# Performance work log

Measured on AMD Instinct MI355X. Metric: run time of the kernel, lower is better.

## Reference

```python
import math
import jax, jax.numpy as jnp
import numpy as np

D_MODEL = 1024
L_MAX = 4096
BATCH = 2
FILTER_ORDER = 64
EMB_DIM = 3


def _make_z(L, emb_dim=EMB_DIM):
    # PositionalEmbedding: [time, real bands, imag bands] -> [1, L, emb_dim]
    t = jnp.linspace(0.0, 1.0, L)[None, :, None]
    bands = (emb_dim - 1) // 2
    t_res = jnp.linspace(0.0, L - 1.0, L)[None, :, None]
    w = 2.0 * math.pi * t_res / L
    f = jnp.linspace(1e-4, float(bands - 1), bands)[None, None]
    ph = f * w  # z = exp(-1j*ph) -> real=cos(ph), imag=-sin(ph)
    return jnp.concatenate([t, jnp.cos(ph), -jnp.sin(ph)], axis=-1).astype(jnp.float32)


def setup_inputs() -> dict:
    key = jax.random.key(0)
    ks = jax.random.split(key, 16)
    d = D_MODEL
    iw = 3 * d  # inner_width = d_model * (order + 1), order=2

    def rn(k, shape, scale):
        return (jax.random.normal(k, shape) * scale).astype(jnp.float32)

    return {
        'u': rn(ks[0], (BATCH, L_MAX, d), 1.0),
        'w_in': rn(ks[1], (iw, d), d ** -0.5),
        'b_in': rn(ks[2], (iw,), 0.01),
        'sf_w': rn(ks[3], (iw, 1, 3), 3 ** -0.5),
        'sf_b': rn(ks[4], (iw,), 0.01),
        'z': _make_z(L_MAX),
        'w0': rn(ks[5], (FILTER_ORDER, EMB_DIM), EMB_DIM ** -0.5),
        'b0': rn(ks[6], (FILTER_ORDER,), 0.01),
        'freq': jnp.ones((1, FILTER_ORDER), dtype=jnp.float32),  # Sin(w=1)
        'w1': rn(ks[7], (FILTER_ORDER, FILTER_ORDER), FILTER_ORDER ** -0.5),
        'b1': rn(ks[8], (FILTER_ORDER,), 0.01),
        'w2': rn(ks[9], (FILTER_ORDER, FILTER_ORDER), FILTER_ORDER ** -0.5),
        'b2': rn(ks[10], (FILTER_ORDER,), 0.01),
        'wf': rn(ks[11], (d, FILTER_ORDER), FILTER_ORDER ** -0.5),
        'D': rn(ks[12], (d,), 1.0),
        'w_out': rn(ks[13], (d, d), d ** -0.5),
        'b_out': rn(ks[14], (d,), 0.01),
    }


def _dwconv(x, w, b):
    # depthwise Conv1d(kernel=3, padding=2, groups=C); x: [B, C, L] -> [B, C, L+2]
    y = jax.lax.conv_general_dilated(
        x, w, window_strides=(1,), padding=[(2, 2)],
        feature_group_count=x.shape[1],
        dimension_numbers=('NCH', 'OIH', 'NCH'))
    return y + b[None, :, None]


def _fftconv(v, k, D):
    # circular conv via zero-padded FFT; torch's k_f/fft_size with norm='forward'
    # irfft cancels to the standard (norm='backward') inverse.
    L = v.shape[-1]
    n = 2 * L
    y = jnp.fft.irfft(jnp.fft.rfft(v, n=n) * jnp.fft.rfft(k, n=n), n=n)[..., :L]
    return y + v * D[:, None]


def reference(u, w_in, b_in, sf_w, sf_b, z, w0, b0, freq, w1, b1, w2, b2, wf, D, w_out, b_out):
    b, l, d = u.shape
    L = min(l, L_MAX)

    # input projection + short depthwise filter
    up = jnp.einsum('bld,ed->ble', u, w_in) + b_in  # [b, l, 3d]
    up = up.transpose(0, 2, 1)                       # [b, 3d, l]
    uc = _dwconv(up, sf_w, sf_b)[..., :L]            # [b, 3d, L]
    x0, x1, v = jnp.split(uc, 3, axis=1)             # each [b, d, L]

    # implicit filter MLP with shared Sin activation
    h = jnp.sin(freq * (z @ w0.T + b0))              # [1, L, 64]
    h = jnp.sin(freq * (h @ w1.T + b1))
    h = jnp.sin(freq * (h @ w2.T + b2))
    h = h @ wf.T                                     # [1, L, d]

    # exponential modulation (buffers: t, deltas)
    t = jnp.linspace(0.0, 1.0, L)[None, :, None]
    max_decay = math.log(0.01) / 0.3
    min_decay = math.log(0.01) / 1.5
    deltas = jnp.linspace(min_decay, max_decay, d)[None, None]
    h = h * jnp.exp(-t * jnp.abs(deltas))            # [1, L, d]
    k = h[0].T                                       # [d, L]

    # hyena recurrence (order=2 -> one gated fft conv)
    v = _fftconv(v * x1, k, D)
    y = (v * x0).transpose(0, 2, 1)                  # [b, L, d]
    return jnp.einsum('bld,ed->ble', y, w_out) + b_out
```

## Files before the change

kernel.cpp:

```cpp
#include <hip/hip_runtime.h>
#include <math.h>

#define DM   1024
#define LL   4096
#define NB   2
#define E3   3072
#define FPI  3.14159265358979323846f

typedef __bf16 bf16x8 __attribute__((ext_vector_type(8)));
typedef float  f32x4  __attribute__((ext_vector_type(4)));
typedef _Float16 f16x2 __attribute__((ext_vector_type(2)));

__device__ __forceinline__ unsigned short f2bf(float x) {
    unsigned u = __float_as_uint(x);
    u += 0x7fffu + ((u >> 16) & 1u);
    return (unsigned short)(u >> 16);
}
__device__ __forceinline__ float bf2f(ushort s) {
    return __uint_as_float(((unsigned)s) << 16);
}
__device__ __forceinline__ void gload16(void* lds, const void* g) {
    typedef const __attribute__((address_space(1))) unsigned int* gp_t;
    typedef __attribute__((address_space(3))) unsigned int* lp_t;
    __builtin_amdgcn_global_load_lds((gp_t)g, (lp_t)lds, 16, 0, 0);
}

__global__ __launch_bounds__(256) void k_cvt3(
    const float* __restrict__ a, ushort* __restrict__ oa, int n4a,
    const float* __restrict__ b, ushort* __restrict__ ob, int n4b,
    const float* __restrict__ c, ushort* __restrict__ oc, int n4c)
{
    int idx = blockIdx.x * 256 + threadIdx.x;
    int stride = gridDim.x * 256;
    int tot = n4a + n4b + n4c;
    for (int i = idx; i < tot; i += stride) {
        const float4* src; ushort* dst; int k;
        if (i < n4a)            { src = (const float4*)a; dst = oa; k = i; }
        else if (i < n4a + n4b) { src = (const float4*)b; dst = ob; k = i - n4a; }
        else                    { src = (const float4*)c; dst = oc; k = i - n4a - n4b; }
        float4 v = src[k];
        ushort4 o;
        o.x = f2bf(v.x); o.y = f2bf(v.y); o.z = f2bf(v.z); o.w = f2bf(v.w);
        *reinterpret_cast<ushort4*>(dst + 4 * k) = o;
    }
}

__global__ __launch_bounds__(512, 1) void k_gemm128n(
    const ushort* __restrict__ A, const ushort* __restrict__ B,
    const float* __restrict__ bias, ushort* __restrict__ C,
    int Ntiles, int ldc)
{
    __shared__ __align__(16) char ldsm[98304];
    const int tid  = threadIdx.x;
    const int lane = tid & 63;
    const int w    = tid >> 6;
    const int wr   = w >> 2, wc = w & 3;

    const int nch = Ntiles >> 3;
    const int xcd = blockIdx.x & 7;
    const int loc = blockIdx.x >> 3;
    const int n0 = ((xcd * nch) + (loc % nch)) << 8;
    const int m0 = (loc / nch) << 7;

    const int r0 = tid >> 2;
    const int swzc = ((tid & 3) ^ ((r0 >> 1) & 3)) << 4;
    const char* Asrc = (const char*)A + ((size_t)(m0 + r0) << 11) + swzc;
    const char* Bsrc = (const char*)B + ((size_t)(n0 + r0) << 11) + swzc;
    char* Ld = ldsm + tid * 16;

    const int lm = lane & 15, lk = lane >> 4;
    const int rA = wr * 64 + lm;
    const int rB = wc * 64 + lm;
    const int aBase = rA * 64 + ((lk ^ ((rA >> 1) & 3)) << 4);
    const int bBase = 16384 + rB * 64 + ((lk ^ ((rB >> 1) & 3)) << 4);

#define STG_A(ks, nb, t1) \
    gload16(Ld + (nb) + (ks)*8192, Asrc + (t1)*128 + (ks)*64)
#define STG_B(ks, nb, t1) do { \
    gload16(Ld + (nb) + 16384 + (ks)*16384,        Bsrc + (t1)*128 + (ks)*64); \
    gload16(Ld + (nb) + 16384 + (ks)*16384 + 8192, Bsrc + (t1)*128 + (ks)*64 + 262144); } while(0)
#define LDA(buf, ks, m) (*(const bf16x8*)(ldsm + (buf) + (ks)*8192 + aBase + (m)*1024))
#define LDB(buf, ks, n) (*(const bf16x8*)(ldsm + (buf) + (ks)*16384 + bBase + (n)*1024))
#define VMCNT3() asm volatile("s_waitcnt vmcnt(3)" ::: "memory")
#define VMCNT0() asm volatile("s_waitcnt vmcnt(0)" ::: "memory")
#define BAR() __builtin_amdgcn_s_barrier()

    f32x4 acc[4][4];
#pragma unroll
    for (int i = 0; i < 4; ++i)
#pragma unroll
        for (int j = 0; j < 4; ++j)
#pragma unroll
            for (int r = 0; r < 4; ++r) acc[i][j][r] = 0.f;

    STG_A(0, 0, 0); STG_B(0, 0, 0); STG_A(1, 0, 0); STG_B(1, 0, 0);
    VMCNT3();
    BAR();

    bf16x8 af[2], bq[4];
#pragma unroll 1
    for (int t = 0; t < 15; ++t) {
        const int buf = (t & 1) * 49152;
        const int nb  = 49152 - buf;
        const int t1  = t + 1;
#pragma unroll
        for (int n = 0; n < 4; ++n) bq[n] = LDB(buf, 0, n);
        af[0] = LDA(buf, 0, 0); af[1] = LDA(buf, 0, 1);
        STG_A(0, nb, t1);
        BAR();
        __builtin_amdgcn_s_setprio(1);
#pragma unroll
        for (int m = 0; m < 2; ++m)
#pragma unroll
            for (int n = 0; n < 4; ++n)
                acc[m][n] = __builtin_amdgcn_mfma_f32_16x16x32_bf16(af[m], bq[n], acc[m][n], 0, 0, 0);
        __builtin_amdgcn_s_setprio(0);
        BAR();
        af[0] = LDA(buf, 0, 2); af[1] = LDA(buf, 0, 3);
        STG_B(0, nb, t1);
        VMCNT3();
        BAR();
        __builtin_amdgcn_s_setprio(1);
#pragma unroll
        for (int m = 0; m < 2; ++m)
#pragma unroll
            for (int n = 0; n < 4; ++n)
                acc[2 + m][n] = __builtin_amdgcn_mfma_f32_16x16x32_bf16(af[m], bq[n], acc[2 + m][n], 0, 0, 0);
        __builtin_amdgcn_s_setprio(0);
        BAR();
#pragma unroll
        for (int n = 0; n < 4; ++n) bq[n] = LDB(buf, 1, n);
        af[0] = LDA(buf, 1, 0); af[1] = LDA(buf, 1, 1);
        STG_A(1, nb, t1);
        BAR();
        __builtin_amdgcn_s_setprio(1);
#pragma unroll
        for (int m = 0; m < 2; ++m)
#pragma unroll
            for (int n = 0; n < 4; ++n)
                acc[m][n] = __builtin_amdgcn_mfma_f32_16x16x32_bf16(af[m], bq[n], acc[m][n], 0, 0, 0);
        __builtin_amdgcn_s_setprio(0);
        BAR();
        af[0] = LDA(buf, 1, 2); af[1] = LDA(buf, 1, 3);
        STG_B(1, nb, t1);
        VMCNT3();
        BAR();
        __builtin_amdgcn_s_setprio(1);
#pragma unroll
        for (int m = 0; m < 2; ++m)
#pragma unroll
            for (int n = 0; n < 4; ++n)
                acc[2 + m][n] = __builtin_amdgcn_mfma_f32_16x16x32_bf16(af[m], bq[n], acc[2 + m][n], 0, 0, 0);
        __builtin_amdgcn_s_setprio(0);
        BAR();
    }
    {
        const int buf = 49152;
#pragma unroll
        for (int n = 0; n < 4; ++n) bq[n] = LDB(buf, 0, n);
        af[0] = LDA(buf, 0, 0); af[1] = LDA(buf, 0, 1);
#pragma unroll
        for (int m = 0; m < 2; ++m)
#pragma unroll
            for (int n = 0; n < 4; ++n)
                acc[m][n] = __builtin_amdgcn_mfma_f32_16x16x32_bf16(af[m], bq[n], acc[m][n], 0, 0, 0);
        af[0] = LDA(buf, 0, 2); af[1] = LDA(buf, 0, 3);
#pragma unroll
        for (int m = 0; m < 2; ++m)
#pragma unroll
            for (int n = 0; n < 4; ++n)
                acc[2 + m][n] = __builtin_amdgcn_mfma_f32_16x16x32_bf16(af[m], bq[n], acc[2 + m][n], 0, 0, 0);
        VMCNT0();
        BAR();
#pragma unroll
        for (int n = 0; n < 4; ++n) bq[n] = LDB(buf, 1, n);
        af[0] = LDA(buf, 1, 0); af[1] = LDA(buf, 1, 1);
#pragma unroll
        for (int m = 0; m < 2; ++m)
#pragma unroll
            for (int n = 0; n < 4; ++n)
                acc[m][n] = __builtin_amdgcn_mfma_f32_16x16x32_bf16(af[m], bq[n], acc[m][n], 0, 0, 0);
        af[0] = LDA(buf, 1, 2); af[1] = LDA(buf, 1, 3);
#pragma unroll
        for (int m = 0; m < 2; ++m)
#pragma unroll
            for (int n = 0; n < 4; ++n)
                acc[2 + m][n] = __builtin_amdgcn_mfma_f32_16x16x32_bf16(af[m], bq[n], acc[2 + m][n], 0, 0, 0);
    }
    const int er = lk << 2, ec = lm;
#pragma unroll
    for (int m = 0; m < 4; ++m) {
        int row = m0 + wr * 64 + m * 16 + er;
#pragma unroll
        for (int n = 0; n < 4; ++n) {
            int col = n0 + wc * 64 + n * 16 + ec;
            ushort* cp = C + (size_t)row * ldc + col;
#pragma unroll
            for (int r = 0; r < 4; ++r)
                cp[(size_t)r * ldc] = f2bf(acc[m][n][r] + bias[row + r]);
        }
    }
#undef STG_A
#undef STG_B
#undef LDA
#undef LDB
#undef VMCNT3
#undef VMCNT0
#undef BAR
}

__global__ __launch_bounds__(256) void k_gemm_bf16(
    const ushort* __restrict__ A, const ushort* __restrict__ B,
    const float* __restrict__ bias, float* __restrict__ C, int ldc)
{
    __shared__ ushort As[128 * 32];
    __shared__ ushort Bs[128 * 32];
    const int tid  = threadIdx.x;
    const int lane = tid & 63;
    const int w    = tid >> 6;
    const int wm   = (w >> 1) << 6, wn = (w & 1) << 6;
    const int m0   = blockIdx.y << 7, n0 = blockIdx.x << 7;

    f32x4 acc[4][4];
#pragma unroll
    for (int i = 0; i < 4; ++i)
#pragma unroll
        for (int j = 0; j < 4; ++j)
#pragma unroll
            for (int r = 0; r < 4; ++r) acc[i][j][r] = 0.f;

    const char* Ab = (const char*)A + ((size_t)(m0 + (tid >> 2)) << 11) + ((tid & 3) << 4);
    const char* Bb = (const char*)B + ((size_t)(n0 + (tid >> 2)) << 11) + ((tid & 3) << 4);
    char* AsD = (char*)As + tid * 16;
    char* BsD = (char*)Bs + tid * 16;
    const char* ap = (const char*)As + ((wm + (lane & 15)) << 6) + ((lane >> 4) << 4);
    const char* bp = (const char*)Bs + ((wn + (lane & 15)) << 6) + ((lane >> 4) << 4);

    for (int k0 = 0; k0 < 1024; k0 += 32) {
        __syncthreads();
        gload16(AsD,        Ab + k0 * 2);
        gload16(AsD + 4096, Ab + 131072 + k0 * 2);
        gload16(BsD,        Bb + k0 * 2);
        gload16(BsD + 4096, Bb + 131072 + k0 * 2);
        __syncthreads();
        bf16x8 af[4], bfr[4];
#pragma unroll
        for (int i = 0; i < 4; ++i) {
            af[i]  = *(const bf16x8*)(ap + (i << 10));
            bfr[i] = *(const bf16x8*)(bp + (i << 10));
        }
#pragma unroll
        for (int i = 0; i < 4; ++i)
#pragma unroll
            for (int j = 0; j < 4; ++j)
                acc[i][j] = __builtin_amdgcn_mfma_f32_16x16x32_bf16(
                    af[i], bfr[j], acc[i][j], 0, 0, 0);
    }
    const int er = (lane >> 4) << 2;
    const int ec = lane & 15;
#pragma unroll
    for (int i = 0; i < 4; ++i) {
        int row = m0 + wm + (i << 4) + er;
#pragma unroll
        for (int j = 0; j < 4; ++j) {
            int col = n0 + wn + (j << 4) + ec;
            float bz = bias[col];
            float* cp = C + (size_t)row * ldc + col;
#pragma unroll
            for (int r = 0; r < 4; ++r)
                cp[(size_t)r * ldc] = acc[i][j][r] + bz;
        }
    }
}

__global__ __launch_bounds__(256) void k_filt_mlp(
    const float* __restrict__ z, const float* __restrict__ w0,
    const float* __restrict__ b0, const float* __restrict__ fr,
    const float* __restrict__ w1, const float* __restrict__ b1,
    const float* __restrict__ w2, const float* __restrict__ b2,
    float* __restrict__ H3)
{
    __shared__ float w1t[64 * 65];
    __shared__ float w2t[64 * 65];
    __shared__ float hb[4][64];
    const int tid = threadIdx.x;
    for (int idx = tid; idx < 4096; idx += 256) {
        int j = idx >> 6, m = idx & 63;
        w1t[m*65 + j] = w1[idx];
        w2t[m*65 + j] = w2[idx];
    }
    __syncthreads();
    const int tl = tid >> 6, j = tid & 63;
    const float frj = fr[j];
    const float b0j = b0[j], b1j = b1[j], b2j = b2[j];
    const float w00 = w0[j*3+0], w01 = w0[j*3+1], w02 = w0[j*3+2];
    const int t0 = blockIdx.x * 16;
    for (int r = 0; r < 4; ++r) {
        int t = t0 + r*4 + tl;
        float z0 = z[t*3+0], z1 = z[t*3+1], z2 = z[t*3+2];
        float h = sinf(frj * (b0j + z0*w00 + z1*w01 + z2*w02));
        hb[tl][j] = h;
        __syncthreads();
        float s = b1j;
#pragma unroll
        for (int m = 0; m < 64; ++m) s = fmaf(hb[tl][m], w1t[m*65 + j], s);
        __syncthreads();
        h = sinf(frj * s);
        hb[tl][j] = h;
        __syncthreads();
        s = b2j;
#pragma unroll
        for (int m = 0; m < 64; ++m) s = fmaf(hb[tl][m], w2t[m*65 + j], s);
        h = sinf(frj * s);
        H3[(size_t)t * 64 + j] = h;
        __syncthreads();
    }
}

__global__ __launch_bounds__(256) void k_filt_k(
    const float* __restrict__ H3, const float* __restrict__ wf,
    float* __restrict__ kf)
{
    __shared__ float Hs[64][65];
    __shared__ float Ws[64][65];
    const int tid = threadIdx.x;
    const int t0 = blockIdx.x * 64, d0 = blockIdx.y * 64;
    for (int idx = tid; idx < 4096; idx += 256) {
        int r = idx >> 6, cc = idx & 63;
        Hs[r][cc] = H3[(size_t)(t0 + r) * 64 + cc];
        Ws[r][cc] = wf[(size_t)(d0 + r) * 64 + cc];
    }
    __syncthreads();
    const int tx = tid & 15, ty = tid >> 4;
    float acc[4][4];
#pragma unroll
    for (int i = 0; i < 4; ++i)
#pragma unroll
        for (int jj = 0; jj < 4; ++jj) acc[i][jj] = 0.f;
#pragma unroll
    for (int j = 0; j < 64; ++j) {
        float wv[4], hv[4];
#pragma unroll
        for (int i = 0; i < 4; ++i) wv[i] = Ws[4*ty + i][j];
#pragma unroll
        for (int i = 0; i < 4; ++i) hv[i] = Hs[4*tx + i][j];
#pragma unroll
        for (int i = 0; i < 4; ++i)
#pragma unroll
            for (int jj = 0; jj < 4; ++jj) acc[i][jj] = fmaf(wv[i], hv[jj], acc[i][jj]);
    }
    const float mind = -3.0701134573253944f;
    const float maxd = -15.350567286626972f;
#pragma unroll
    for (int i = 0; i < 4; ++i) {
        int d = d0 + 4*ty + i;
        float delta = fabsf(mind + (maxd - mind) * ((float)d / 1023.f));
#pragma unroll
        for (int jj = 0; jj < 4; ++jj) {
            int t = t0 + 4*tx + jj;
            float tn = (float)t / 4095.f;
            kf[(size_t)d * LL + t] = acc[i][jj] * expf(-tn * delta);
        }
    }
}

__device__ __forceinline__ int pidx(int p) { return p + (p >> 4); }

__device__ __forceinline__ float2 cmul(float2 a, float2 b) {
    return make_float2(a.x*b.x - a.y*b.y, a.x*b.y + a.y*b.x);
}

__device__ void fft_lds_fwd4(float2* buf, int tid) {
    int lh = 10;
#pragma unroll
    for (int h = 2048; h >= 32; h >>= 2, lh -= 2) {
        const int hh = h >> 1;
        const float rinv = -FPI / (float)h;
        __syncthreads();
#pragma unroll
        for (int r = 0; r < 4; ++r) {
            int bf = (r << 9) + tid;
            int q  = bf & (hh - 1);
            int g  = bf >> lh;
            int j  = (g << (lh + 2)) + q;
            float2 a = buf[pidx(j)];
            float2 b = buf[pidx(j + hh)];
            float2 c = buf[pidx(j + h)];
            float2 d = buf[pidx(j + h + hh)];
            float2 t0 = make_float2(a.x + c.x, a.y + c.y);
            float2 t1 = make_float2(a.x - c.x, a.y - c.y);
            float2 t2 = make_float2(b.x + d.x, b.y + d.y);
            float2 t3 = make_float2(b.y - d.y, d.x - b.x);
            float sn, cs;
            __sincosf(rinv * (float)q, &sn, &cs);
            float c2 = cs*cs - sn*sn, s2 = 2.f*cs*sn;
            float c3 = cs*c2 - sn*s2, s3 = cs*s2 + sn*c2;
            buf[pidx(j)] = make_float2(t0.x + t2.x, t0.y + t2.y);
            float2 e1 = make_float2(t0.x - t2.x, t0.y - t2.y);
            buf[pidx(j + hh)] = make_float2(e1.x*c2 - e1.y*s2, e1.x*s2 + e1.y*c2);
            float2 e2 = make_float2(t1.x + t3.x, t1.y + t3.y);
            buf[pidx(j + h)] = make_float2(e2.x*cs - e2.y*sn, e2.x*sn + e2.y*cs);
            float2 e3 = make_float2(t1.x - t3.x, t1.y - t3.y);
            buf[pidx(j + h + hh)] = make_float2(e3.x*c3 - e3.y*s3, e3.x*s3 + e3.y*c3);
        }
    }
    __syncthreads();
}

__device__ void fft_lds_inv4(float2* buf, int tid) {
    int lh = 4;
#pragma unroll
    for (int h = 32; h <= 2048; h <<= 2, lh += 2) {
        const int hh = h >> 1;
        const float rpos = FPI / (float)h;
        __syncthreads();
#pragma unroll
        for (int r = 0; r < 4; ++r) {
            int bf = (r << 9) + tid;
            int q  = bf & (hh - 1);
            int g  = bf >> lh;
            int j  = (g << (lh + 2)) + q;
            float2 o0 = buf[pidx(j)];
            float2 o1 = buf[pidx(j + hh)];
            float2 o2 = buf[pidx(j + h)];
            float2 o3 = buf[pidx(j + h + hh)];
            float sn, cs;
            __sincosf(rpos * (float)q, &sn, &cs);
            float c2 = cs*cs - sn*sn, s2 = 2.f*cs*sn;
            float c3 = cs*c2 - sn*s2, s3 = cs*s2 + sn*c2;
            float2 p1 = make_float2(o1.x*c2 - o1.y*s2, o1.x*s2 + o1.y*c2);
            float2 p2 = make_float2(o2.x*cs - o2.y*sn, o2.x*sn + o2.y*cs);
            float2 p3 = make_float2(o3.x*c3 - o3.y*s3, o3.x*s3 + o3.y*c3);
            float2 u0 = make_float2(o0.x + p1.x, o0.y + p1.y);
            float2 u1 = make_float2(o0.x - p1.x, o0.y - p1.y);
            float2 u2 = make_float2(p2.x + p3.x, p2.y + p3.y);
            float2 u3 = make_float2(p2.x - p3.x, p2.y - p3.y);
            float2 ib = make_float2(-u3.y, u3.x);
            buf[pidx(j)]          = make_float2(u0.x + u2.x, u0.y + u2.y);
            buf[pidx(j + hh)]     = make_float2(u1.x + ib.x, u1.y + ib.y);
            buf[pidx(j + h)]      = make_float2(u0.x - u2.x, u0.y - u2.y);
            buf[pidx(j + h + hh)] = make_float2(u1.x - ib.x, u1.y - ib.y);
        }
    }
    __syncthreads();
}

__device__ __forceinline__ void fft_reg_fwd(float2* c) {
    const float W16r[8] = {1.f, 0.92387953f, 0.70710678f, 0.38268343f,
                           0.f, -0.38268343f, -0.70710678f, -0.92387953f};
    const float W16i[8] = {0.f, -0.38268343f, -0.70710678f, -0.92387953f,
                           -1.f, -0.92387953f, -0.70710678f, -0.38268343f};
#pragma unroll
    for (int k = 0; k < 8; ++k) {
        float2 a = c[k], b = c[k+8];
        float2 d = make_float2(a.x - b.x, a.y - b.y);
        c[k]   = make_float2(a.x + b.x, a.y + b.y);
        c[k+8] = cmul(d, make_float2(W16r[k], W16i[k]));
    }
    const float W8r[4] = {1.f, 0.70710678f, 0.f, -0.70710678f};
    const float W8i[4] = {0.f, -0.70710678f, -1.f, -0.70710678f};
#pragma unroll
    for (int blk = 0; blk < 16; blk += 8)
#pragma unroll
        for (int k = 0; k < 4; ++k) {
            float2 a = c[blk+k], b = c[blk+k+4];
            float2 d = make_float2(a.x - b.x, a.y - b.y);
            c[blk+k]   = make_float2(a.x + b.x, a.y + b.y);
            c[blk+k+4] = cmul(d, make_float2(W8r[k], W8i[k]));
        }
#pragma unroll
    for (int blk = 0; blk < 16; blk += 4) {
        {   float2 a = c[blk], b = c[blk+2];
            c[blk]   = make_float2(a.x + b.x, a.y + b.y);
            c[blk+2] = make_float2(a.x - b.x, a.y - b.y); }
        {   float2 a = c[blk+1], b = c[blk+3];
            float2 d = make_float2(a.x - b.x, a.y - b.y);
            c[blk+1] = make_float2(a.x + b.x, a.y + b.y);
            c[blk+3] = make_float2(d.y, -d.x); }
    }
#pragma unroll
    for (int blk = 0; blk < 16; blk += 2) {
        float2 a = c[blk], b = c[blk+1];
        c[blk]   = make_float2(a.x + b.x, a.y + b.y);
        c[blk+1] = make_float2(a.x - b.x, a.y - b.y);
    }
}

__device__ __forceinline__ void fft_reg_inv(float2* c) {
#pragma unroll
    for (int blk = 0; blk < 16; blk += 2) {
        float2 a = c[blk], b = c[blk+1];
        c[blk]   = make_float2(a.x + b.x, a.y + b.y);
        c[blk+1] = make_float2(a.x - b.x, a.y - b.y);
    }
#pragma unroll
    for (int blk = 0; blk < 16; blk += 4) {
        {   float2 a = c[blk], b = c[blk+2];
            c[blk]   = make_float2(a.x + b.x, a.y + b.y);
            c[blk+2] = make_float2(a.x - b.x, a.y - b.y); }
        {   float2 a = c[blk+1], b = c[blk+3];
            float2 bt = make_float2(-c[blk+3].y, c[blk+3].x);
            c[blk+1] = make_float2(a.x + bt.x, a.y + bt.y);
            c[blk+3] = make_float2(a.x - bt.x, a.y - bt.y); }
    }
    const float W8r[4] = {1.f, 0.70710678f, 0.f, -0.70710678f};
    const float W8i[4] = {0.f, 0.70710678f, 1.f, 0.70710678f};
#pragma unroll
    for (int blk = 0; blk < 16; blk += 8)
#pragma unroll
        for (int k = 0; k < 4; ++k) {
            float2 a = c[blk+k], b = c[blk+k+4];
            float2 bt = cmul(b, make_float2(W8r[k], W8i[k]));
            c[blk+k]   = make_float2(a.x + bt.x, a.y + bt.y);
            c[blk+k+4] = make_float2(a.x - bt.x, a.y - bt.y);
        }
    const float W16r[8] = {1.f, 0.92387953f, 0.70710678f, 0.38268343f,
                           0.f, -0.38268343f, -0.70710678f, -0.92387953f};
    const float W16i[8] = {0.f, 0.38268343f, 0.70710678f, 0.92387953f,
                           1.f, 0.92387953f, 0.70710678f, 0.38268343f};
#pragma unroll
    for (int k = 0; k < 8; ++k) {
        float2 a = c[k], b = c[k+8];
        float2 bt = cmul(b, make_float2(W16r[k], W16i[k]));
        c[k]   = make_float2(a.x + bt.x, a.y + bt.y);
        c[k+8] = make_float2(a.x - bt.x, a.y - bt.y);
    }
}

__global__ __launch_bounds__(512) void k_kfft(
    const float* __restrict__ kf, f16x2* __restrict__ Kf)
{
    __shared__ float2 buf[8704];
    const int d = blockIdx.x, tid = threadIdx.x;
    const float* krow = kf + (size_t)d * LL;
    const float rinv0 = -FPI / 4096.f;
    for (int i = tid; i < 1024; i += 512) {
        float4 k4 = reinterpret_cast<const float4*>(krow)[i];
        int p = 4 * i;
        float kv[4] = {k4.x, k4.y, k4.z, k4.w};
#pragma unroll
        for (int q = 0; q < 4; ++q) {
            float sn, cs;
            __sincosf(rinv0 * (float)(p + q), &sn, &cs);
            buf[pidx(p + q)]        = make_float2(kv[q], 0.f);
            buf[pidx(p + q + 4096)] = make_float2(kv[q] * cs, kv[q] * sn);
        }
    }
    fft_lds_fwd4(buf, tid);
    float2 c[16];
    const int p0 = tid * 16;
#pragma unroll
    for (int j = 0; j < 16; ++j) c[j] = buf[pidx(p0 + j)];
    fft_reg_fwd(c);
    f16x2* outp = Kf + (size_t)d * 8192 + p0;
#pragma unroll
    for (int j = 0; j < 16; ++j) {
        f16x2 o;
        o[0] = (_Float16)(c[j].x * (1.f/8192.f));
        o[1] = (_Float16)(c[j].y * (1.f/8192.f));
        outp[j] = o;
    }
}

__device__ __forceinline__ void conv4(const ushort* __restrict__ row, int p,
    float w0, float w1, float w2, float bias, float* out)
{
    float xm2, xm1;
    if (p >= 2) {
        unsigned prev = *reinterpret_cast<const unsigned*>(row + p - 2);
        xm2 = bf2f((ushort)(prev & 0xffffu));
        xm1 = bf2f((ushort)(prev >> 16));
    } else { xm2 = 0.f; xm1 = 0.f; }
    uint2 cur = *reinterpret_cast<const uint2*>(row + p);
    float x0 = bf2f((ushort)(cur.x & 0xffffu));
    float x1 = bf2f((ushort)(cur.x >> 16));
    float x2 = bf2f((ushort)(cur.y & 0xffffu));
    float x3 = bf2f((ushort)(cur.y >> 16));
    out[0] = fmaf(w2, x0, fmaf(w1, xm1, fmaf(w0, xm2, bias)));
    out[1] = fmaf(w2, x1, fmaf(w1, x0,  fmaf(w0, xm1, bias)));
    out[2] = fmaf(w2, x2, fmaf(w1, x1,  fmaf(w0, x0,  bias)));
    out[3] = fmaf(w2, x3, fmaf(w1, x2,  fmaf(w0, x1,  bias)));
}

__global__ __launch_bounds__(512) void k_fftconv(
    const ushort* __restrict__ up2, const f16x2* __restrict__ Kf,
    const float* __restrict__ sfw, const float* __restrict__ sfb,
    const float* __restrict__ Dp, ushort* __restrict__ yg)
{
    __shared__ float2 buf[8704];
    const int d = blockIdx.x, tid = threadIdx.x;
    const ushort* vrow0  = up2 + (size_t)(2048 + d) * 8192;
    const ushort* vrow1  = vrow0 + 4096;
    const ushort* x1row0 = up2 + (size_t)(1024 + d) * 8192;
    const ushort* x1row1 = x1row0 + 4096;
    const ushort* x0row0 = up2 + (size_t)d * 8192;
    const ushort* x0row1 = x0row0 + 4096;
    const float wv0 = sfw[(2048+d)*3+0], wv1 = sfw[(2048+d)*3+1],
                wv2 = sfw[(2048+d)*3+2], bv = sfb[2048+d];
    const float wx0 = sfw[(1024+d)*3+0], wx1 = sfw[(1024+d)*3+1],
                wx2 = sfw[(1024+d)*3+2], bx = sfb[1024+d];
    const float g0 = sfw[d*3+0], g1 = sfw[d*3+1], g2 = sfw[d*3+2], bg = sfb[d];
    const float rinv0 = -FPI / 4096.f;

    float vs0[8], vs1[8];
#pragma unroll
    for (int ii = 0; ii < 2; ++ii) {
        int p = 4 * tid + ii * 2048;
        float cv0[4], cv1[4], cx0[4], cx1[4];
        conv4(vrow0,  p, wv0, wv1, wv2, bv, cv0);
        conv4(vrow1,  p, wv0, wv1, wv2, bv, cv1);
        conv4(x1row0, p, wx0, wx1, wx2, bx, cx0);
        conv4(x1row1, p, wx0, wx1, wx2, bx, cx1);
#pragma unroll
        for (int q = 0; q < 4; ++q) {
            float z0 = cv0[q] * cx0[q];
            float z1 = cv1[q] * cx1[q];
            vs0[ii*4 + q] = z0;
            vs1[ii*4 + q] = z1;
            float sn, cs;
            __sincosf(rinv0 * (float)(p + q), &sn, &cs);
            float2 z = make_float2(z0, z1);
            buf[pidx(p + q)]        = z;
            buf[pidx(p + q + 4096)] = cmul(z, make_float2(cs, sn));
        }
    }
    fft_lds_fwd4(buf, tid);
    float2 c[16];
    const int p0 = tid * 16;
#pragma unroll
    for (int j = 0; j < 16; ++j) c[j] = buf[pidx(p0 + j)];
    fft_reg_fwd(c);
    const f16x2* kfr = Kf + (size_t)d * 8192 + p0;
#pragma unroll
    for (int j = 0; j < 16; ++j) {
        f16x2 kv = kfr[j];
        c[j] = cmul(c[j], make_float2((float)kv[0], (float)kv[1]));
    }
    fft_reg_inv(c);
#pragma unroll
    for (int j = 0; j < 16; ++j) buf[pidx(p0 + j)] = c[j];
    fft_lds_inv4(buf, tid);
    const float Dd = Dp[d];
    ushort* orow0 = yg + (size_t)d * LL;
    ushort* orow1 = yg + ((size_t)DM + d) * LL;
    const float rinv4 = FPI / 4096.f;
#pragma unroll
    for (int ii = 0; ii < 2; ++ii) {
        int p = 4 * tid + ii * 2048;
        float cg0[4], cg1[4];
        conv4(x0row0, p, g0, g1, g2, bg, cg0);
        conv4(x0row1, p, g0, g1, g2, bg, cg1);
        ushort s0[4], s1[4];
#pragma unroll
        for (int q = 0; q < 4; ++q) {
            float sn, cs;
            __sincosf(rinv4 * (float)(p + q), &sn, &cs);
            float2 a  = buf[pidx(p + q)];
            float2 bb = buf[pidx(p + q + 4096)];
            float2 bt = cmul(bb, make_float2(cs, sn));
            s0[q] = f2bf((a.x + bt.x + Dd * vs0[ii*4 + q]) * cg0[q]);
            s1[q] = f2bf((a.y + bt.y + Dd * vs1[ii*4 + q]) * cg1[q]);
        }
        *reinterpret_cast<ushort4*>(orow0 + p) = make_ushort4(s0[0], s0[1], s0[2], s0[3]);
        *reinterpret_cast<ushort4*>(orow1 + p) = make_ushort4(s1[0], s1[1], s1[2], s1[3]);
    }
}

__global__ __launch_bounds__(256) void k_tr(
    const ushort* __restrict__ yg, ushort* __restrict__ Ag)
{
    __shared__ ushort S[64][72];
    const int b  = blockIdx.z;
    const int d0 = blockIdx.y * 64;
    const int t0 = blockIdx.x * 64;
    const int tid = threadIdx.x;
#pragma unroll
    for (int p = 0; p < 2; ++p) {
        int idx = p * 256 + tid;
        int dr = idx >> 3, c8 = (idx & 7) << 3;
        uint4 v = *reinterpret_cast<const uint4*>(
            yg + ((size_t)b * DM + d0 + dr) * LL + t0 + c8);
        *reinterpret_cast<uint4*>(&S[dr][c8]) = v;
    }
    __syncthreads();
#pragma unroll
    for (int p = 0; p < 2; ++p) {
        int idx = p * 256 + tid;
        int tr = idx >> 3, dq = (idx & 7) << 3;
        ushort tmp[8] __attribute__((aligned(16)));
#pragma unroll
        for (int q = 0; q < 8; ++q) tmp[q] = S[dq + q][tr];
        *reinterpret_cast<uint4*>(Ag + ((size_t)b * LL + t0 + tr) * DM + d0 + dq) =
            *reinterpret_cast<uint4*>(tmp);
    }
}

extern "C" void kernel_launch(void* const* d_in, const int* in_sizes, int n_in,
                              void* d_out, int out_size, void* d_ws, size_t ws_size,
                              hipStream_t stream)
{
    if (n_in < 17) return;
    const float* u    = (const float*)d_in[0];
    const float* w_in = (const float*)d_in[1];
    const float* b_in = (const float*)d_in[2];
    const float* sf_w = (const float*)d_in[3];
    const float* sf_b = (const float*)d_in[4];
    const float* z    = (const float*)d_in[5];
    const float* w0   = (const float*)d_in[6];
    const float* b0   = (const float*)d_in[7];
    const float* freq = (const float*)d_in[8];
    const float* w1   = (const float*)d_in[9];
    const float* b1   = (const float*)d_in[10];
    const float* w2   = (const float*)d_in[11];
    const float* b2   = (const float*)d_in[12];
    const float* wf   = (const float*)d_in[13];
    const float* Dp   = (const float*)d_in[14];
    const float* wout = (const float*)d_in[15];
    const float* bout = (const float*)d_in[16];
    float* out = (float*)d_out;
    float* ws  = (float*)d_ws;

    ushort* up2   = (ushort*)ws;
    float*  kfbuf = ws + 16777216;
    ushort* yg    = (ushort*)(ws + 16777216);
    float*  H3    = ws + 20971520;
    ushort* Ag    = (ushort*)(ws + 20971520);
    ushort* ub    = (ushort*)(ws + 25165824);
    ushort* wb    = (ushort*)(ws + 33554432);
    f16x2*  Kf    = (f16x2*)(ws + 33554432);
    ushort* woutb = (ushort*)(ws + 41943040);
    const size_t NEED = (size_t)(41943040 + 524288) * 4;
    if (ws_size < NEED) return;

    hipLaunchKernelGGL(k_cvt3,     dim3(2048), dim3(256), 0, stream,
                       u, ub, 2097152, w_in, wb, 786432, wout, woutb, 262144);
    hipLaunchKernelGGL(k_gemm128n, dim3((E3/128) * (8192/256)), dim3(512), 0, stream,
                       wb, ub, b_in, up2, 8192/256, 8192);
    hipLaunchKernelGGL(k_filt_mlp, dim3(LL/16), dim3(256), 0, stream,
                       z, w0, b0, freq, w1, b1, w2, b2, H3);
    hipLaunchKernelGGL(k_filt_k,   dim3(LL/64, DM/64), dim3(256), 0, stream,
                       H3, wf, kfbuf);
    hipLaunchKernelGGL(k_kfft,     dim3(DM), dim3(512), 0, stream,
                       kfbuf, Kf);
    hipLaunchKernelGGL(k_fftconv,  dim3(DM), dim3(512), 0, stream,
                       up2, Kf, sf_w, sf_b, Dp, yg);
    hipLaunchKernelGGL(k_tr,       dim3(LL/64, DM/64, NB), dim3(256), 0, stream,
                       yg, Ag);
    hipLaunchKernelGGL(k_gemm_bf16, dim3(DM/128, 8192/128), dim3(256), 0, stream,
                       Ag, woutb, bout, out, DM);
}
```

Measured before the change: 219.9 us.

## Replace radix-4 LDS FFT passes with radix-8 passes to cut barriers and LDS traffic

The shared-memory FFT stages move from four radix-4 passes plus a radix-2 step in registers to three radix-8 passes, with the in-register stage shrunk from 16-point to 8-point sub-FFTs. This lowers the number of block-wide barriers and LDS read/write round trips per 8192-point FFT in both the filter FFT and the main conv kernel. Twiddles are computed once per pass per thread instead of per butterfly. The cost is higher register pressure, since each thread holds eight complex values per butterfly.

After: 247.4 us. 12.5% more time.

```diff
diff --git a/kernel.cpp b/kernel.cpp
--- a/kernel.cpp
+++ b/kernel.cpp
@@ -6,6 +6,7 @@
 #define NB   2
 #define E3   3072
 #define FPI  3.14159265358979323846f
+#define RCQ  0.70710678118654752f
 
 typedef __bf16 bf16x8 __attribute__((ext_vector_type(8)));
 typedef float  f32x4  __attribute__((ext_vector_type(4)));
@@ -369,94 +370,125 @@
 __device__ __forceinline__ float2 cmul(float2 a, float2 b) {
     return make_float2(a.x*b.x - a.y*b.y, a.x*b.y + a.y*b.x);
 }
-
-__device__ void fft_lds_fwd4(float2* buf, int tid) {
-    int lh = 10;
-#pragma unroll
-    for (int h = 2048; h >= 32; h >>= 2, lh -= 2) {
-        const int hh = h >> 1;
-        const float rinv = -FPI / (float)h;
-        __syncthreads();
-#pragma unroll
-        for (int r = 0; r < 4; ++r) {
-            int bf = (r << 9) + tid;
-            int q  = bf & (hh - 1);
-            int g  = bf >> lh;
-            int j  = (g << (lh + 2)) + q;
-            float2 a = buf[pidx(j)];
-            float2 b = buf[pidx(j + hh)];
-            float2 c = buf[pidx(j + h)];
-            float2 d = buf[pidx(j + h + hh)];
-            float2 t0 = make_float2(a.x + c.x, a.y + c.y);
-            float2 t1 = make_float2(a.x - c.x, a.y - c.y);
-            float2 t2 = make_float2(b.x + d.x, b.y + d.y);
-            float2 t3 = make_float2(b.y - d.y, d.x - b.x);
-            float sn, cs;
-            __sincosf(rinv * (float)q, &sn, &cs);
-            float c2 = cs*cs - sn*sn, s2 = 2.f*cs*sn;
-            float c3 = cs*c2 - sn*s2, s3 = cs*s2 + sn*c2;
-            buf[pidx(j)] = make_float2(t0.x + t2.x, t0.y + t2.y);
-            float2 e1 = make_float2(t0.x - t2.x, t0.y - t2.y);
-            buf[pidx(j + hh)] = make_float2(e1.x*c2 - e1.y*s2, e1.x*s2 + e1.y*c2);
-            float2 e2 = make_float2(t1.x + t3.x, t1.y + t3.y);
-            buf[pidx(j + h)] = make_float2(e2.x*cs - e2.y*sn, e2.x*sn + e2.y*cs);
-            float2 e3 = make_float2(t1.x - t3.x, t1.y - t3.y);
-            buf[pidx(j + h + hh)] = make_float2(e3.x*c3 - e3.y*s3, e3.x*s3 + e3.y*c3);
-        }
-    }
+__device__ __forceinline__ float2 cadd(float2 a, float2 b) {
+    return make_float2(a.x + b.x, a.y + b.y);
+}
+__device__ __forceinline__ float2 csub(float2 a, float2 b) {
+    return make_float2(a.x - b.x, a.y - b.y);
+}
+__device__ __forceinline__ float2 cmulni(float2 a) {
+    return make_float2(a.y, -a.x);
+}
+__device__ __forceinline__ float2 cmulpi(float2 a) {
+    return make_float2(-a.y, a.x);
+}
+
+__device__ __forceinline__ void r8f_pass(float2* buf, int tid, int h, int lh) {
+    const int hh = h >> 2;
+    const float rinv = -FPI / (float)h;
+    const int q = tid & (hh - 1);
+    float sn, cs;
+    __sincosf(rinv * (float)q, &sn, &cs);
+    float2 w  = make_float2(cs, sn);
+    float2 wc = make_float2((cs + sn)*RCQ, (sn - cs)*RCQ);
+    float2 w2 = cmul(w, w);
+    float2 w4 = cmul(w2, w2);
     __syncthreads();
-}
-
-__device__ void fft_lds_inv4(float2* buf, int tid) {
-    int lh = 4;
-#pragma unroll
-    for (int h = 32; h <= 2048; h <<= 2, lh += 2) {
-        const int hh = h >> 1;
-        const float rpos = FPI / (float)h;
-        __syncthreads();
-#pragma unroll
-        for (int r = 0; r < 4; ++r) {
-            int bf = (r << 9) + tid;
-            int q  = bf & (hh - 1);
-            int g  = bf >> lh;
-            int j  = (g << (lh + 2)) + q;
-            float2 o0 = buf[pidx(j)];
-            float2 o1 = buf[pidx(j + hh)];
-            float2 o2 = buf[pidx(j + h)];
-            float2 o3 = buf[pidx(j + h + hh)];
-            float sn, cs;
-            __sincosf(rpos * (float)q, &sn, &cs);
-            float c2 = cs*cs - sn*sn, s2 = 2.f*cs*sn;
-            float c3 = cs*c2 - sn*s2, s3 = cs*s2 + sn*c2;
-            float2 p1 = make_float2(o1.x*c2 - o1.y*s2, o1.x*s2 + o1.y*c2);
-            float2 p2 = make_float2(o2.x*cs - o2.y*sn, o2.x*sn + o2.y*cs);
-            float2 p3 = make_float2(o3.x*c3 - o3.y*s3, o3.x*s3 + o3.y*c3);
-            float2 u0 = make_float2(o0.x + p1.x, o0.y + p1.y);
-            float2 u1 = make_float2(o0.x - p1.x, o0.y - p1.y);
-            float2 u2 = make_float2(p2.x + p3.x, p2.y + p3.y);
-            float2 u3 = make_float2(p2.x - p3.x, p2.y - p3.y);
-            float2 ib = make_float2(-u3.y, u3.x);
-            buf[pidx(j)]          = make_float2(u0.x + u2.x, u0.y + u2.y);
-            buf[pidx(j + hh)]     = make_float2(u1.x + ib.x, u1.y + ib.y);
-            buf[pidx(j + h)]      = make_float2(u0.x - u2.x, u0.y - u2.y);
-            buf[pidx(j + h + hh)] = make_float2(u1.x - ib.x, u1.y - ib.y);
-        }
-    }
+#pragma unroll
+    for (int r = 0; r < 2; ++r) {
+        int bf = tid + (r << 9);
+        int g  = bf >> lh;
+        int j  = (g << (lh + 3)) + q;
+        float2 x0 = buf[pidx(j)];
+        float2 x1 = buf[pidx(j + hh)];
+        float2 x2 = buf[pidx(j + 2*hh)];
+        float2 x3 = buf[pidx(j + 3*hh)];
+        float2 x4 = buf[pidx(j + 4*hh)];
+        float2 x5 = buf[pidx(j + 5*hh)];
+        float2 x6 = buf[pidx(j + 6*hh)];
+        float2 x7 = buf[pidx(j + 7*hh)];
+        float2 u0 = cadd(x0, x4), u1 = cadd(x1, x5);
+        float2 u2 = cadd(x2, x6), u3 = cadd(x3, x7);
+        float2 v0 = cmul(csub(x0, x4), w);
+        float2 v1 = cmul(csub(x1, x5), wc);
+        float2 v2 = cmulni(cmul(csub(x2, x6), w));
+        float2 v3 = cmulni(cmul(csub(x3, x7), wc));
+        float2 A0 = cadd(u0, u2), A1 = cadd(u1, u3);
+        float2 B0 = cmul(csub(u0, u2), w2);
+        float2 B1 = cmulni(cmul(csub(u1, u3), w2));
+        float2 C0 = cadd(v0, v2), C1 = cadd(v1, v3);
+        float2 D0 = cmul(csub(v0, v2), w2);
+        float2 D1 = cmulni(cmul(csub(v1, v3), w2));
+        buf[pidx(j)]        = cadd(A0, A1);
+        buf[pidx(j + hh)]   = cmul(csub(A0, A1), w4);
+        buf[pidx(j + 2*hh)] = cadd(B0, B1);
+        buf[pidx(j + 3*hh)] = cmul(csub(B0, B1), w4);
+        buf[pidx(j + 4*hh)] = cadd(C0, C1);
+        buf[pidx(j + 5*hh)] = cmul(csub(C0, C1), w4);
+        buf[pidx(j + 6*hh)] = cadd(D0, D1);
+        buf[pidx(j + 7*hh)] = cmul(csub(D0, D1), w4);
+    }
+}
+
+__device__ __forceinline__ void r8i_pass(float2* buf, int tid, int h, int lh) {
+    const int hh = h >> 2;
+    const float rpos = FPI / (float)h;
+    const int q = tid & (hh - 1);
+    float sn, cs;
+    __sincosf(rpos * (float)q, &sn, &cs);
+    float2 w  = make_float2(cs, sn);
+    float2 wc = make_float2((cs - sn)*RCQ, (sn + cs)*RCQ);
+    float2 w2 = cmul(w, w);
+    float2 w4 = cmul(w2, w2);
     __syncthreads();
+#pragma unroll
+    for (int r = 0; r < 2; ++r) {
+        int bf = tid + (r << 9);
+        int g  = bf >> lh;
+        int j  = (g << (lh + 3)) + q;
+        float2 y0 = buf[pidx(j)];
+        float2 y1 = buf[pidx(j + hh)];
+        float2 y2 = buf[pidx(j + 2*hh)];
+        float2 y3 = buf[pidx(j + 3*hh)];
+        float2 y4 = buf[pidx(j + 4*hh)];
+        float2 y5 = buf[pidx(j + 5*hh)];
+        float2 y6 = buf[pidx(j + 6*hh)];
+        float2 y7 = buf[pidx(j + 7*hh)];
+        float2 s;
+        s = cmul(y1, w4); float2 A0 = cadd(y0, s), A1 = csub(y0, s);
+        s = cmul(y3, w4); float2 B0 = cadd(y2, s), B1 = csub(y2, s);
+        s = cmul(y5, w4); float2 C0 = cadd(y4, s), C1 = csub(y4, s);
+        s = cmul(y7, w4); float2 D0 = cadd(y6, s), D1 = csub(y6, s);
+        s = cmul(B0, w2);          float2 u0 = cadd(A0, s), u2 = csub(A0, s);
+        s = cmulpi(cmul(B1, w2));  float2 u1 = cadd(A1, s), u3 = csub(A1, s);
+        s = cmul(D0, w2);          float2 v0 = cadd(C0, s), v2 = csub(C0, s);
+        s = cmulpi(cmul(D1, w2));  float2 v1 = cadd(C1, s), v3 = csub(C1, s);
+        s = cmul(v0, w);           buf[pidx(j)]        = cadd(u0, s);
+                                   buf[pidx(j + 4*hh)] = csub(u0, s);
+        s = cmul(v1, wc);          buf[pidx(j + hh)]   = cadd(u1, s);
+                                   buf[pidx(j + 5*hh)] = csub(u1, s);
+        s = cmulpi(cmul(v2, w));   buf[pidx(j + 2*hh)] = cadd(u2, s);
+                                   buf[pidx(j + 6*hh)] = csub(u2, s);
+        s = cmulpi(cmul(v3, wc));  buf[pidx(j + 3*hh)] = cadd(u3, s);
+                                   buf[pidx(j + 7*hh)] = csub(u3, s);
+    }
+}
+
+__device__ void fft_lds_fwd8(float2* buf, int tid) {
+    r8f_pass(buf, tid, 2048, 9);
+    r8f_pass(buf, tid, 256, 6);
+    r8f_pass(buf, tid, 32, 3);
+    __syncthreads();
+}
+
+__device__ void fft_lds_inv8(float2* buf, int tid) {
+    r8i_pass(buf, tid, 32, 3);
+    r8i_pass(buf, tid, 256, 6);
+    r8i_pass(buf, tid, 2048, 9);
+    __syncthreads();
 }
 
 __device__ __forceinline__ void fft_reg_fwd(float2* c) {
-    const float W16r[8] = {1.f, 0.92387953f, 0.70710678f, 0.38268343f,
-                           0.f, -0.38268343f, -0.70710678f, -0.92387953f};
-    const float W16i[8] = {0.f, -0.38268343f, -0.70710678f, -0.92387953f,
-                           -1.f, -0.92387953f, -0.70710678f, -0.38268343f};
-#pragma unroll
-    for (int k = 0; k < 8; ++k) {
-        float2 a = c[k], b = c[k+8];
-        float2 d = make_float2(a.x - b.x, a.y - b.y);
-        c[k]   = make_float2(a.x + b.x, a.y + b.y);
-        c[k+8] = cmul(d, make_float2(W16r[k], W16i[k]));
-    }
     const float W8r[4] = {1.f, 0.70710678f, 0.f, -0.70710678f};
     const float W8i[4] = {0.f, -0.70710678f, -1.f, -0.70710678f};
 #pragma unroll
@@ -464,25 +496,25 @@
 #pragma unroll
         for (int k = 0; k < 4; ++k) {
             float2 a = c[blk+k], b = c[blk+k+4];
-            float2 d = make_float2(a.x - b.x, a.y - b.y);
-            c[blk+k]   = make_float2(a.x + b.x, a.y + b.y);
+            float2 d = csub(a, b);
+            c[blk+k]   = cadd(a, b);
             c[blk+k+4] = cmul(d, make_float2(W8r[k], W8i[k]));
         }
 #pragma unroll
     for (int blk = 0; blk < 16; blk += 4) {
         {   float2 a = c[blk], b = c[blk+2];
-            c[blk]   = make_float2(a.x + b.x, a.y + b.y);
-            c[blk+2] = make_float2(a.x - b.x, a.y - b.y); }
+            c[blk]   = cadd(a, b);
+            c[blk+2] = csub(a, b); }
         {   float2 a = c[blk+1], b = c[blk+3];
-            float2 d = make_float2(a.x - b.x, a.y - b.y);
-            c[blk+1] = make_float2(a.x + b.x, a.y + b.y);
+            float2 d = csub(a, b);
+            c[blk+1] = cadd(a, b);
             c[blk+3] = make_float2(d.y, -d.x); }
     }
 #pragma unroll
     for (int blk = 0; blk < 16; blk += 2) {
         float2 a = c[blk], b = c[blk+1];
-        c[blk]   = make_float2(a.x + b.x, a.y + b.y);
-        c[blk+1] = make_float2(a.x - b.x, a.y - b.y);
+        c[blk]   = cadd(a, b);
+        c[blk+1] = csub(a, b);
     }
 }
 
@@ -490,18 +522,18 @@
 #pragma unroll
     for (int blk = 0; blk < 16; blk += 2) {
         float2 a = c[blk], b = c[blk+1];
-        c[blk]   = make_float2(a.x + b.x, a.y + b.y);
-        c[blk+1] = make_float2(a.x - b.x, a.y - b.y);
+        c[blk]   = cadd(a, b);
+        c[blk+1] = csub(a, b);
     }
 #pragma unroll
     for (int blk = 0; blk < 16; blk += 4) {
         {   float2 a = c[blk], b = c[blk+2];
-            c[blk]   = make_float2(a.x + b.x, a.y + b.y);
-            c[blk+2] = make_float2(a.x - b.x, a.y - b.y); }
+            c[blk]   = cadd(a, b);
+            c[blk+2] = csub(a, b); }
         {   float2 a = c[blk+1], b = c[blk+3];
             float2 bt = make_float2(-c[blk+3].y, c[blk+3].x);
-            c[blk+1] = make_float2(a.x + bt.x, a.y + bt.y);
-            c[blk+3] = make_float2(a.x - bt.x, a.y - bt.y); }
+            c[blk+1] = cadd(a, bt);
+            c[blk+3] = csub(a, bt); }
     }
     const float W8r[4] = {1.f, 0.70710678f, 0.f, -0.70710678f};
     const float W8i[4] = {0.f, 0.70710678f, 1.f, 0.70710678f};
@@ -511,20 +543,9 @@
         for (int k = 0; k < 4; ++k) {
             float2 a = c[blk+k], b = c[blk+k+4];
             float2 bt = cmul(b, make_float2(W8r[k], W8i[k]));
-            c[blk+k]   = make_float2(a.x + bt.x, a.y + bt.y);
-            c[blk+k+4] = make_float2(a.x - bt.x, a.y - bt.y);
-        }
-    const float W16r[8] = {1.f, 0.92387953f, 0.70710678f, 0.38268343f,
-                           0.f, -0.38268343f, -0.70710678f, -0.92387953f};
-    const float W16i[8] = {0.f, 0.38268343f, 0.70710678f, 0.92387953f,
-                           1.f, 0.92387953f, 0.70710678f, 0.38268343f};
-#pragma unroll
-    for (int k = 0; k < 8; ++k) {
-        float2 a = c[k], b = c[k+8];
-        float2 bt = cmul(b, make_float2(W16r[k], W16i[k]));
-        c[k]   = make_float2(a.x + bt.x, a.y + bt.y);
-        c[k+8] = make_float2(a.x - bt.x, a.y - bt.y);
-    }
+            c[blk+k]   = cadd(a, bt);
+            c[blk+k+4] = csub(a, bt);
+        }
 }
 
 __global__ __launch_bounds__(512) void k_kfft(
@@ -546,7 +567,7 @@
             buf[pidx(p + q + 4096)] = make_float2(kv[q] * cs, kv[q] * sn);
         }
     }
-    fft_lds_fwd4(buf, tid);
+    fft_lds_fwd8(buf, tid);
     float2 c[16];
     const int p0 = tid * 16;
 #pragma unroll
@@ -624,7 +645,7 @@
             buf[pidx(p + q + 4096)] = cmul(z, make_float2(cs, sn));
         }
     }
-    fft_lds_fwd4(buf, tid);
+    fft_lds_fwd8(buf, tid);
     float2 c[16];
     const int p0 = tid * 16;
 #pragma unroll
@@ -639,7 +660,7 @@
     fft_reg_inv(c);
 #pragma unroll
     for (int j = 0; j < 16; ++j) buf[pidx(p0 + j)] = c[j];
-    fft_lds_inv4(buf, tid);
+    fft_lds_inv8(buf, tid);
     const float Dd = Dp[d];
     ushort* orow0 = yg + (size_t)d * LL;
     ushort* orow1 = yg + ((size_t)DM + d) * LL;
```
